# Kernel tuning notes

Hardware: AMD Instinct MI355X
Metric: run time of the kernel (lower is better)

## Reference

```python
import jax, jax.numpy as jnp
import numpy as np
from jax import lax

# ---- static config (matches init_kwargs) ----
B, D, H, HD, MLP = 64, 768, 12, 64, 3072
DEPTH = 11                     # trunk blocks; block 12 is used (twice) as b1/b2
IMG_H, IMG_W, P, S = 256, 128, 16, 12
NY, NX = (IMG_H - P) // S + 1, (IMG_W - P) // S + 1   # 21, 10
NP = NY * NX                   # 210 patches
N = NP + 1                     # +CLS = 211 tokens
NUM_CIDS = 8
SCALE = HD ** -0.5
SIE = 3.0                      # sie_xishu
SHIFT, GROUPS, DIV = 5, 2, 4
EPS = 1e-6
_PNAMES = ["ln1_g", "ln1_b", "qkv_w", "qkv_b", "proj_w", "proj_b",
           "ln2_g", "ln2_b", "fc1_w", "fc1_b", "fc2_w", "fc2_b"]


def layernorm(x, g, b):
    m = jnp.mean(x, -1, keepdims=True)
    v = jnp.mean(jnp.square(x - m), -1, keepdims=True)
    return (x - m) * lax.rsqrt(v + EPS) * g + b


def block(x, p):
    """Pre-norm ViT block: manual attention (q@k.T softmax @v) + GELU MLP."""
    ln1g, ln1b, qkvw, qkvb, projw, projb, ln2g, ln2b, fc1w, fc1b, fc2w, fc2b = p
    Bn, Nn = x.shape[0], x.shape[1]
    h = layernorm(x, ln1g, ln1b)
    qkv = (h @ qkvw + qkvb).reshape(Bn, Nn, 3, H, HD)
    q, k, v = qkv[:, :, 0], qkv[:, :, 1], qkv[:, :, 2]           # [B,N,H,HD]
    attn = jax.nn.softmax(jnp.einsum('bnhd,bmhd->bhnm', q * SCALE, k), axis=-1)
    o = jnp.einsum('bhnm,bmhd->bnhd', attn, v).reshape(Bn, Nn, D)
    x = x + o @ projw + projb
    h = layernorm(x, ln2g, ln2b)
    return x + jax.nn.gelu(h @ fc1w + fc1b, approximate=False) @ fc2w + fc2b


def _block_params(k, lead=()):
    ks = jax.random.split(k, 4)
    z = lambda s: jnp.zeros(lead + s, jnp.float32)
    o = lambda s: jnp.ones(lead + s, jnp.float32)
    r = lambda kk, s, fan: jax.random.normal(kk, lead + s, jnp.float32) * (fan ** -0.5)
    return dict(ln1_g=o((D,)), ln1_b=z((D,)),
                qkv_w=r(ks[0], (D, 3 * D), D), qkv_b=z((3 * D,)),
                proj_w=r(ks[1], (D, D), D), proj_b=z((D,)),
                ln2_g=o((D,)), ln2_b=z((D,)),
                fc1_w=r(ks[2], (D, MLP), D), fc1_b=z((MLP,)),
                fc2_w=r(ks[3], (MLP, D), MLP), fc2_b=z((D,)))


def setup_inputs() -> dict:
    key = jax.random.key(0)
    k = jax.random.split(key, 8)
    inp = {
        "x": jax.random.normal(k[0], (B, 3, IMG_H, IMG_W), jnp.float32),
        "cids": jax.random.randint(k[1], (B,), 0, NUM_CIDS),
        "conv_w": jax.random.normal(k[2], (D, 3, P, P), jnp.float32) * np.float32(np.sqrt(2.0 / (P * P * D))),
        "conv_b": jnp.zeros((D,), jnp.float32),
        "cls_token": jax.random.normal(k[3], (1, 1, D), jnp.float32) * 0.02,
        "pos_embed": jax.random.normal(k[4], (1, N, D), jnp.float32) * 0.02,
        "sie_embed": jax.random.normal(k[5], (NUM_CIDS, 1, D), jnp.float32) * 0.02,
    }
    for name, arr in _block_params(k[6], (DEPTH,)).items():
        inp["blk_" + name] = arr
    for pre, kk in (("b1_", jax.random.fold_in(key, 101)), ("b2_", jax.random.fold_in(key, 102))):
        for name, arr in _block_params(kk).items():
            inp[pre + name] = arr
        inp[pre + "norm_g"] = jnp.ones((D,), jnp.float32)
        inp[pre + "norm_b"] = jnp.zeros((D,), jnp.float32)
    return inp


def reference(x, cids, conv_w, conv_b, cls_token, pos_embed, sie_embed,
              blk_ln1_g, blk_ln1_b, blk_qkv_w, blk_qkv_b, blk_proj_w, blk_proj_b,
              blk_ln2_g, blk_ln2_b, blk_fc1_w, blk_fc1_b, blk_fc2_w, blk_fc2_b,
              b1_ln1_g, b1_ln1_b, b1_qkv_w, b1_qkv_b, b1_proj_w, b1_proj_b,
              b1_ln2_g, b1_ln2_b, b1_fc1_w, b1_fc1_b, b1_fc2_w, b1_fc2_b,
              b1_norm_g, b1_norm_b,
              b2_ln1_g, b2_ln1_b, b2_qkv_w, b2_qkv_b, b2_proj_w, b2_proj_b,
              b2_ln2_g, b2_ln2_b, b2_fc1_w, b2_fc1_b, b2_fc2_w, b2_fc2_b,
              b2_norm_g, b2_norm_b):
    Bn = x.shape[0]
    # overlapping patch embed: Conv2d(3->768, k=16, s=12), flatten, transpose
    y = lax.conv_general_dilated(x, conv_w, (S, S), 'VALID',
                                 dimension_numbers=('NCHW', 'OIHW', 'NCHW'))
    y = (y + conv_b[None, :, None, None]).reshape(Bn, D, NP).transpose(0, 2, 1)
    t = jnp.concatenate([jnp.broadcast_to(cls_token, (Bn, 1, D)), y], axis=1)
    t = t + pos_embed + SIE * sie_embed[cids]   # SIE camera embedding
    # 11 trunk blocks via scan over stacked params
    stk = (blk_ln1_g, blk_ln1_b, blk_qkv_w, blk_qkv_b, blk_proj_w, blk_proj_b,
           blk_ln2_g, blk_ln2_b, blk_fc1_w, blk_fc1_b, blk_fc2_w, blk_fc2_b)
    t = lax.scan(lambda c, p: (block(c, p), None), t, stk)[0]
    # global branch: b1 = block12 + final norm, take CLS
    b1p = (b1_ln1_g, b1_ln1_b, b1_qkv_w, b1_qkv_b, b1_proj_w, b1_proj_b,
           b1_ln2_g, b1_ln2_b, b1_fc1_w, b1_fc1_b, b1_fc2_w, b1_fc2_b)
    f0 = layernorm(block(t, b1p), b1_norm_g, b1_norm_b)[:, 0]
    # shuffle_unit(t, shift=5, group=2, begin=1) -> jigsaw rearranged patches [B,210,D]
    xs = jnp.concatenate([t[:, SHIFT:], t[:, 1:SHIFT]], axis=1)
    xs = xs.reshape(Bn, GROUPS, -1, D).transpose(0, 2, 1, 3).reshape(Bn, -1, D)
    token = t[:, 0:1]
    pl = NP // DIV                                   # 52
    b2p = (b2_ln1_g, b2_ln1_b, b2_qkv_w, b2_qkv_b, b2_proj_w, b2_proj_b,
           b2_ln2_g, b2_ln2_b, b2_fc1_w, b2_fc1_b, b2_fc2_w, b2_fc2_b)
    feats = [f0]
    for i in range(DIV):
        seg = jnp.concatenate([token, xs[:, i * pl:(i + 1) * pl]], axis=1)   # [B,53,D]
        feats.append(layernorm(block(seg, b2p), b2_norm_g, b2_norm_b)[:, 0])
    # eval output with neck_feat='before': necks pass features through;
    # concat global + local/divide_length -> [B, 5*768]
    return jnp.concatenate([feats[0]] + [f / DIV for f in feats[1:]], axis=1)
```

## Files before the change

kernel.cpp:

```cpp
#include <hip/hip_runtime.h>
#include <hip/hip_bf16.h>
#include <cstdint>
#include <cstddef>
#include <math.h>

using bf16 = __hip_bfloat16;
typedef __bf16 bf16x8 __attribute__((ext_vector_type(8)));
typedef float f32x4 __attribute__((ext_vector_type(4)));

static constexpr int NHEAD = 12;
static constexpr int NTOK  = 211;
static constexpr int DEPTH = 11;

static __device__ __forceinline__ void gload_lds16(const bf16* g, bf16* lds) {
  __builtin_amdgcn_global_load_lds(
      (const __attribute__((address_space(1))) uint32_t*)g,
      (__attribute__((address_space(3))) uint32_t*)lds,
      16, 0, 0);
}

__device__ __forceinline__ float gelu_f(float x) {
  float u = x * (0.7978845608f + 0.0356774081f * x * x);
  float t = 1.f - 2.f / (__expf(2.f * u) + 1.f);
  return 0.5f * x * (1.f + t);
}

static __device__ __forceinline__ unsigned short bf16_bits(float x) {
  return __builtin_bit_cast(unsigned short, __float2bfloat16(x));
}

template <bool GELU, bool RES, typename CT>
__global__ __launch_bounds__(256) void gemm_db(
    const bf16* __restrict__ A, const bf16* __restrict__ Bt,
    const float* __restrict__ bias, const float* __restrict__ res,
    CT* __restrict__ C, int M, int N, int K, int gn)
{
  __shared__ bf16 sb[2][8192];

  const int tid = threadIdx.x;
  const int w = tid >> 6, l = tid & 63;
  const int lr = l & 15, lg = l >> 4;
  const int wr = (w >> 1) * 64, wc = (w & 1) * 64;

  const int nwg = gridDim.x, lin = blockIdx.x;
  const int q = nwg >> 3, r = nwg & 7;
  const int xcd = lin & 7, pos = lin >> 3;
  const int wg = (xcd < r ? xcd * (q + 1) : r * (q + 1) + (xcd - r) * q) + pos;
  const int bm0 = (wg / gn) * 128, bn0 = (wg % gn) * 128;

  f32x4 acc[4][4];
#pragma unroll
  for (int i = 0; i < 4; ++i)
#pragma unroll
    for (int j = 0; j < 4; ++j) acc[i][j] = f32x4{0.f, 0.f, 0.f, 0.f};

  size_t aof[2], bof[2]; int dst[2];
#pragma unroll
  for (int j = 0; j < 2; ++j) {
    const int c = j * 256 + tid;
    const int row = c >> 2;
    const int ch = (c & 3) ^ ((row >> 1) & 3);
    int ar = bm0 + row; if (ar >= M) ar = M - 1;
    aof[j] = (size_t)ar * K + ch * 8;
    bof[j] = (size_t)(bn0 + row) * K + ch * 8;
    dst[j] = c * 8;
  }

  const int nt = K >> 5;

  auto stage = [&](int t) {
    bf16* s = sb[t & 1];
    const size_t ko = (size_t)t * 32;
    gload_lds16(A + aof[0] + ko, s + dst[0]);
    gload_lds16(A + aof[1] + ko, s + dst[1]);
    gload_lds16(Bt + bof[0] + ko, s + 4096 + dst[0]);
    gload_lds16(Bt + bof[1] + ko, s + 4096 + dst[1]);
  };

  stage(0);
  __syncthreads();

  const int swz = (lg ^ ((lr >> 1) & 3)) * 8;

  for (int t = 0; t < nt; ++t) {
    if (t + 1 < nt) stage(t + 1);
    const bf16* As = sb[t & 1];
    const bf16* Bs = As + 4096;
    bf16x8 af[4], bv[4];
#pragma unroll
    for (int mi = 0; mi < 4; ++mi)
      af[mi] = *(const bf16x8*)(As + (wr + mi * 16 + lr) * 32 + swz);
#pragma unroll
    for (int ni = 0; ni < 4; ++ni)
      bv[ni] = *(const bf16x8*)(Bs + (wc + ni * 16 + lr) * 32 + swz);
#pragma unroll
    for (int mi = 0; mi < 4; ++mi)
#pragma unroll
      for (int ni = 0; ni < 4; ++ni)
        acc[mi][ni] = __builtin_amdgcn_mfma_f32_16x16x32_bf16(af[mi], bv[ni], acc[mi][ni], 0, 0, 0);
    __syncthreads();
  }

  if constexpr (sizeof(CT) == 2) {
    char* lb = (char*)sb;
#pragma unroll
    for (int mi = 0; mi < 4; ++mi) {
#pragma unroll
      for (int ni = 0; ni < 4; ++ni) {
        const int cloc = wc + ni * 16 + lr;
        const float bvl = bias[bn0 + cloc];
#pragma unroll
        for (int r2 = 0; r2 < 4; ++r2) {
          const int rowl = wr + mi * 16 + lg * 4 + r2;
          float v = acc[mi][ni][r2] + bvl;
          if constexpr (GELU) v = gelu_f(v);
          *(unsigned short*)(lb + rowl * 256 + ((cloc * 2) ^ (((rowl >> 1) & 6) << 4))) =
              bf16_bits(v);
        }
      }
    }
    __syncthreads();
#pragma unroll
    for (int j = 0; j < 8; ++j) {
      const int flat = j * 256 + tid;
      const int row = flat >> 4, ch = flat & 15;
      const int grow = bm0 + row;
      if (grow < M) {
        const f32x4 v = *(const f32x4*)(lb + row * 256 + ((ch * 16) ^ (((row >> 1) & 6) << 4)));
        *(f32x4*)((char*)C + ((size_t)grow * N + bn0 + ch * 8) * 2) = v;
      }
    }
  } else {
#pragma unroll
    for (int mi = 0; mi < 4; ++mi) {
#pragma unroll
      for (int ni = 0; ni < 4; ++ni) {
        const int col = bn0 + wc + ni * 16 + lr;
        const float bvl = bias[col];
#pragma unroll
        for (int r2 = 0; r2 < 4; ++r2) {
          const int row = bm0 + wr + mi * 16 + lg * 4 + r2;
          if (row < M) {
            float v = acc[mi][ni][r2] + bvl;
            if constexpr (GELU) v = gelu_f(v);
            if constexpr (RES) v += res[(size_t)row * N + col];
            C[(size_t)row * N + col] = v;
          }
        }
      }
    }
  }
}

__global__ __launch_bounds__(256) void vtrans_kernel(
    const bf16* __restrict__ qkv, bf16* __restrict__ vT, int ntok, int pad)
{
  __shared__ unsigned short t[224 * 65];
  const int bb = blockIdx.x, h = blockIdx.y;
  const unsigned short* src = (const unsigned short*)qkv + (size_t)bb * ntok * 2304 + 1536 + h * 64;
  for (int idx = threadIdx.x; idx < ntok * 64; idx += 256) {
    int tok = idx >> 6, d = idx & 63;
    t[tok * 65 + d] = src[(size_t)tok * 2304 + d];
  }
  __syncthreads();
  unsigned short* dst = (unsigned short*)vT + (size_t)(bb * 12 + h) * 64 * pad;
  for (int idx = threadIdx.x; idx < 64 * ntok; idx += 256) {
    int d = idx / ntok, tok = idx - d * ntok;
    dst[(size_t)d * pad + tok] = t[tok * 65 + d];
  }
}

template <int NKF>
__global__ __launch_bounds__(256) void attn_kernel(
    const bf16* __restrict__ qkv, const bf16* __restrict__ vT,
    bf16* __restrict__ ao, int ntok, int pad)
{
  constexpr int NPAD = NKF * 16;
  __shared__ bf16 Pl[4][16][NPAD];
  const int bb = blockIdx.x;
  const int h = blockIdx.y;
  const int tid = threadIdx.x;
  const int w = tid >> 6, l = tid & 63;
  const int lr = l & 15, lg = l >> 4;
  const __bf16* base = reinterpret_cast<const __bf16*>(qkv) + (size_t)bb * ntok * 2304 + h * 64;
  const __bf16* vt = reinterpret_cast<const __bf16*>(vT) + (size_t)(bb * 12 + h) * 64 * pad;

  for (int qt = w; qt < NKF; qt += 4) {
    int qrow = qt * 16 + lr; if (qrow >= ntok) qrow = ntok - 1;
    const __bf16* qp = base + (size_t)qrow * 2304 + lg * 8;
    const bf16x8 qf0 = *reinterpret_cast<const bf16x8*>(qp);
    const bf16x8 qf1 = *reinterpret_cast<const bf16x8*>(qp + 32);

    f32x4 s[NKF];
#pragma unroll
    for (int kf = 0; kf < NKF; ++kf) {
      int krow = kf * 16 + lr; if (krow >= ntok) krow = ntok - 1;
      const __bf16* kp = base + (size_t)krow * 2304 + 768 + lg * 8;
      f32x4 a = f32x4{0.f, 0.f, 0.f, 0.f};
      a = __builtin_amdgcn_mfma_f32_16x16x32_bf16(qf0, *reinterpret_cast<const bf16x8*>(kp), a, 0, 0, 0);
      a = __builtin_amdgcn_mfma_f32_16x16x32_bf16(qf1, *reinterpret_cast<const bf16x8*>(kp + 32), a, 0, 0, 0);
      s[kf] = a;
    }

    float rs[4];
#pragma unroll
    for (int r = 0; r < 4; ++r) {
      float mx = -1e30f;
#pragma unroll
      for (int kf = 0; kf < NKF; ++kf)
        if (kf * 16 + lr < ntok) mx = fmaxf(mx, s[kf][r]);
#pragma unroll
      for (int d = 1; d < 16; d <<= 1) mx = fmaxf(mx, __shfl_xor(mx, d));
      float sum = 0.f;
#pragma unroll
      for (int kf = 0; kf < NKF; ++kf) {
        float p = 0.f;
        if (kf * 16 + lr < ntok) p = __expf((s[kf][r] - mx) * 0.125f);
        sum += p;
        Pl[w][lg * 4 + r][kf * 16 + lr] = __float2bfloat16(p);
      }
#pragma unroll
      for (int d = 1; d < 16; d <<= 1) sum += __shfl_xor(sum, d);
      rs[r] = sum;
    }
    __builtin_amdgcn_s_waitcnt(0);

    f32x4 o[4];
#pragma unroll
    for (int ni = 0; ni < 4; ++ni) o[ni] = f32x4{0.f, 0.f, 0.f, 0.f};
#pragma unroll
    for (int ks = 0; ks < NPAD / 32; ++ks) {
      const bf16x8 pa = *reinterpret_cast<const bf16x8*>(&Pl[w][lr][ks * 32 + lg * 8]);
#pragma unroll
      for (int ni = 0; ni < 4; ++ni) {
        const bf16x8 vb = *reinterpret_cast<const bf16x8*>(
            vt + (size_t)(ni * 16 + lr) * pad + ks * 32 + lg * 8);
        o[ni] = __builtin_amdgcn_mfma_f32_16x16x32_bf16(pa, vb, o[ni], 0, 0, 0);
      }
    }
#pragma unroll
    for (int ni = 0; ni < 4; ++ni)
#pragma unroll
      for (int r = 0; r < 4; ++r) {
        int qq = qt * 16 + lg * 4 + r;
        if (qq < ntok) {
          float val = o[ni][r] / rs[r];
          ao[((size_t)bb * ntok + qq) * 768 + h * 64 + ni * 16 + lr] = __float2bfloat16(val);
        }
      }
  }
}

__global__ __launch_bounds__(256) void ln_kernel(
    const float* __restrict__ x, const float* __restrict__ g, const float* __restrict__ b,
    bf16* __restrict__ out, int Mrows)
{
  int row = blockIdx.x * 4 + (threadIdx.x >> 6);
  if (row >= Mrows) return;
  int l = threadIdx.x & 63;
  const float4* xr = reinterpret_cast<const float4*>(x + (size_t)row * 768);
  float4 v[3]; float s = 0.f;
#pragma unroll
  for (int i = 0; i < 3; ++i) {
    v[i] = xr[l + i * 64];
    s += v[i].x + v[i].y + v[i].z + v[i].w;
  }
#pragma unroll
  for (int d = 1; d < 64; d <<= 1) s += __shfl_xor(s, d);
  float mean = s * (1.f / 768.f);
  float s2 = 0.f;
#pragma unroll
  for (int i = 0; i < 3; ++i) {
    float a0 = v[i].x - mean, a1 = v[i].y - mean, a2 = v[i].z - mean, a3 = v[i].w - mean;
    s2 += a0 * a0 + a1 * a1 + a2 * a2 + a3 * a3;
  }
#pragma unroll
  for (int d = 1; d < 64; d <<= 1) s2 += __shfl_xor(s2, d);
  float rstd = rsqrtf(s2 * (1.f / 768.f) + 1e-6f);
  const float4* g4 = reinterpret_cast<const float4*>(g);
  const float4* b4 = reinterpret_cast<const float4*>(b);
  unsigned short* orow = reinterpret_cast<unsigned short*>(out + (size_t)row * 768);
#pragma unroll
  for (int i = 0; i < 3; ++i) {
    float4 gg = g4[l + i * 64], bb = b4[l + i * 64];
    ushort4 pk;
    pk.x = bf16_bits((v[i].x - mean) * rstd * gg.x + bb.x);
    pk.y = bf16_bits((v[i].y - mean) * rstd * gg.y + bb.y);
    pk.z = bf16_bits((v[i].z - mean) * rstd * gg.z + bb.z);
    pk.w = bf16_bits((v[i].w - mean) * rstd * gg.w + bb.w);
    *reinterpret_cast<ushort4*>(orow + (l + i * 64) * 4) = pk;
  }
}

__global__ __launch_bounds__(256) void ln_head_kernel(
    const float* __restrict__ x, int tokstride, const float* __restrict__ g,
    const float* __restrict__ b, float* __restrict__ out, int nbb, int mode)
{
  int bb = blockIdx.x * 4 + (threadIdx.x >> 6);
  if (bb >= nbb) return;
  int l = threadIdx.x & 63;
  const float* xr = x + (size_t)bb * tokstride * 768;
  float v[12]; float s = 0.f;
#pragma unroll
  for (int i = 0; i < 12; ++i) { v[i] = xr[l + i * 64]; s += v[i]; }
#pragma unroll
  for (int d = 1; d < 64; d <<= 1) s += __shfl_xor(s, d);
  float mean = s * (1.f / 768.f);
  float s2 = 0.f;
#pragma unroll
  for (int i = 0; i < 12; ++i) { float t = v[i] - mean; s2 += t * t; }
#pragma unroll
  for (int d = 1; d < 64; d <<= 1) s2 += __shfl_xor(s2, d);
  float rstd = rsqrtf(s2 * (1.f / 768.f) + 1e-6f);
  float scale = mode ? 0.25f : 1.f;
  int b_ = mode ? (bb & 63) : bb;
  int off = mode ? (1 + (bb >> 6)) * 768 : 0;
  float* orow = out + (size_t)b_ * 3840 + off;
#pragma unroll
  for (int i = 0; i < 12; ++i) {
    orow[l + i * 64] = ((v[i] - mean) * rstd * g[l + i * 64] + b[l + i * 64]) * scale;
  }
}

__global__ __launch_bounds__(256) void transpose4_k(
    const float* __restrict__ w0, const float* __restrict__ w1,
    const float* __restrict__ w2, const float* __restrict__ w3,
    bf16* __restrict__ d0, bf16* __restrict__ d1,
    bf16* __restrict__ d2, bf16* __restrict__ d3)
{
  __shared__ float tile[32][33];
  int id = blockIdx.x;
  const float* in; bf16* out; int R, C, tt;
  if (id < 1728)      { in = w0; out = d0; R = 768;  C = 2304; tt = id; }
  else if (id < 2304) { in = w1; out = d1; R = 768;  C = 768;  tt = id - 1728; }
  else if (id < 4608) { in = w2; out = d2; R = 768;  C = 3072; tt = id - 2304; }
  else                { in = w3; out = d3; R = 3072; C = 768;  tt = id - 4608; }
  const int tc = C >> 5;
  int c0 = (tt % tc) * 32, r0 = (tt / tc) * 32;
  int tx = threadIdx.x & 31, ty = threadIdx.x >> 5;
#pragma unroll
  for (int i = 0; i < 4; ++i) {
    int rr = ty + i * 8;
    tile[rr][tx] = in[(size_t)(r0 + rr) * C + c0 + tx];
  }
  __syncthreads();
#pragma unroll
  for (int i = 0; i < 4; ++i) {
    int c = ty + i * 8;
    out[(size_t)(c0 + c) * R + r0 + tx] = __float2bfloat16(tile[tx][c]);
  }
}

__global__ void cast_kernel(const float* __restrict__ in, bf16* __restrict__ out, int n)
{
  int idx = blockIdx.x * 256 + threadIdx.x;
  if (idx < n) out[idx] = __float2bfloat16(in[idx]);
}

__global__ void im2col_kernel(const float* __restrict__ x, bf16* __restrict__ pm)
{
  int idx = blockIdx.x * 256 + threadIdx.x;
  if (idx >= 13440 * 768) return;
  int k = idx % 768;
  int m = idx / 768;
  int b = m / 210, p = m % 210;
  int py = p / 10, px = p % 10;
  int c = k >> 8, ij = k & 255, i = ij >> 4, j = ij & 15;
  pm[idx] = __float2bfloat16(x[(((size_t)b * 3 + c) * 256 + py * 12 + i) * 128 + px * 12 + j]);
}

__global__ void assemble_kernel(
    const bf16* __restrict__ y, const float* __restrict__ cls, const float* __restrict__ pos,
    const float* __restrict__ sie, const int* __restrict__ cids, float* __restrict__ tA)
{
  int idx = blockIdx.x * 256 + threadIdx.x;
  if (idx >= 13504 * 768) return;
  int d = idx % 768;
  int t = (idx / 768) % 211;
  int b = idx / (768 * 211);
  float v = pos[t * 768 + d] + 3.0f * sie[cids[b] * 768 + d];
  if (t == 0) v += cls[d];
  else v += __bfloat162float(y[((size_t)b * 210 + (t - 1)) * 768 + d]);
  tA[idx] = v;
}

__global__ void gather_kernel(const float* __restrict__ tA, float* __restrict__ tB)
{
  int idx = blockIdx.x * 256 + threadIdx.x;
  if (idx >= 256 * 53 * 768) return;
  int d = idx % 768;
  int jj = (idx / 768) % 53;
  int bb = idx / (768 * 53);
  int i = bb >> 6, b = bb & 63;
  int src;
  if (jj == 0) src = 0;
  else {
    int jx = i * 52 + (jj - 1);
    int mm = (jx & 1) * 105 + (jx >> 1);
    src = (mm < 206) ? (5 + mm) : (1 + (mm - 206));
  }
  tB[idx] = tA[((size_t)b * 211 + src) * 768 + d];
}

struct BlkP {
  const float *ln1_g, *ln1_b, *qkv_w, *qkv_b, *proj_w, *proj_b;
  const float *ln2_g, *ln2_b, *fc1_w, *fc1_b, *fc2_w, *fc2_b;
};

extern "C" void kernel_launch(void* const* d_in, const int* in_sizes, int n_in,
                              void* d_out, int out_size, void* d_ws, size_t ws_size,
                              hipStream_t stream)
{
  (void)in_sizes; (void)n_in; (void)out_size; (void)ws_size;
  const float* xin   = (const float*)d_in[0];
  const int*   cids  = (const int*)  d_in[1];
  const float* convw = (const float*)d_in[2];
  const float* convb = (const float*)d_in[3];
  const float* cls   = (const float*)d_in[4];
  const float* pos   = (const float*)d_in[5];
  const float* sie   = (const float*)d_in[6];
  float* out = (float*)d_out;

  char* ws = (char*)d_ws;
  bf16*  qkvT = (bf16*)(ws + 0);
  bf16*  projT = (bf16*)(ws + 3538944);
  bf16*  fc1T = (bf16*)(ws + 4718592);
  bf16*  fc2T = (bf16*)(ws + 9437184);
  float* tA   = (float*)(ws + 14155776);
  float* tB   = (float*)(ws + 55640064);
  bf16*  hb   = (bf16*)(ws + 97320960);
  bf16*  big  = (bf16*)(ws + 118161408);
  bf16*  ao   = (bf16*)(ws + 201523200);
  bf16*  vTb  = (bf16*)(ws + 222363648);

  dim3 blk(256);

  auto apply_block = [&](float* xbuf, const BlkP& p, int nb, int ntok_) {
    const int M = nb * ntok_;
    const int gm = (M + 127) / 128;
    const int pad = (ntok_ == NTOK) ? 224 : 64;
    transpose4_k<<<dim3(6912), blk, 0, stream>>>(
        p.qkv_w, p.proj_w, p.fc1_w, p.fc2_w, qkvT, projT, fc1T, fc2T);
    ln_kernel<<<dim3((M + 3) / 4), blk, 0, stream>>>(xbuf, p.ln1_g, p.ln1_b, hb, M);
    gemm_db<false, false, bf16><<<dim3(gm * 18), blk, 0, stream>>>(
        hb, qkvT, p.qkv_b, nullptr, big, M, 2304, 768, 18);
    vtrans_kernel<<<dim3(nb, NHEAD), blk, 0, stream>>>(big, vTb, ntok_, pad);
    if (ntok_ == NTOK)
      attn_kernel<14><<<dim3(nb, NHEAD), blk, 0, stream>>>(big, vTb, ao, ntok_, pad);
    else
      attn_kernel<4><<<dim3(nb, NHEAD), blk, 0, stream>>>(big, vTb, ao, ntok_, pad);
    gemm_db<false, true, float><<<dim3(gm * 6), blk, 0, stream>>>(
        ao, projT, p.proj_b, xbuf, xbuf, M, 768, 768, 6);
    ln_kernel<<<dim3((M + 3) / 4), blk, 0, stream>>>(xbuf, p.ln2_g, p.ln2_b, hb, M);
    gemm_db<true, false, bf16><<<dim3(gm * 24), blk, 0, stream>>>(
        hb, fc1T, p.fc1_b, nullptr, big, M, 3072, 768, 24);
    gemm_db<false, true, float><<<dim3(gm * 6), blk, 0, stream>>>(
        big, fc2T, p.fc2_b, xbuf, xbuf, M, 768, 3072, 6);
  };

  {
    int total = 13440 * 768;
    im2col_kernel<<<dim3((total + 255) / 256), blk, 0, stream>>>(xin, big);
    int nw = 768 * 768;
    cast_kernel<<<dim3((nw + 255) / 256), blk, 0, stream>>>(convw, qkvT, nw);
    gemm_db<false, false, bf16><<<dim3(105 * 6), blk, 0, stream>>>(
        big, qkvT, convb, nullptr, ao, 13440, 768, 768, 6);
    total = 13504 * 768;
    assemble_kernel<<<dim3((total + 255) / 256), blk, 0, stream>>>(ao, cls, pos, sie, cids, tA);
  }

  const float* bp[12];
  for (int i = 0; i < 12; ++i) bp[i] = (const float*)d_in[7 + i];
  for (int dd = 0; dd < DEPTH; ++dd) {
    BlkP p;
    p.ln1_g = bp[0] + dd * 768;                p.ln1_b = bp[1] + dd * 768;
    p.qkv_w = bp[2] + (size_t)dd * 768 * 2304; p.qkv_b = bp[3] + dd * 2304;
    p.proj_w = bp[4] + (size_t)dd * 768 * 768; p.proj_b = bp[5] + dd * 768;
    p.ln2_g = bp[6] + dd * 768;                p.ln2_b = bp[7] + dd * 768;
    p.fc1_w = bp[8] + (size_t)dd * 768 * 3072; p.fc1_b = bp[9] + dd * 3072;
    p.fc2_w = bp[10] + (size_t)dd * 3072 * 768; p.fc2_b = bp[11] + dd * 768;
    apply_block(tA, p, 64, NTOK);
  }

  (void)hipMemcpyAsync(tB, tA, (size_t)13504 * 768 * 4, hipMemcpyDeviceToDevice, stream);
  {
    BlkP p;
    p.ln1_g = (const float*)d_in[19]; p.ln1_b = (const float*)d_in[20];
    p.qkv_w = (const float*)d_in[21]; p.qkv_b = (const float*)d_in[22];
    p.proj_w = (const float*)d_in[23]; p.proj_b = (const float*)d_in[24];
    p.ln2_g = (const float*)d_in[25]; p.ln2_b = (const float*)d_in[26];
    p.fc1_w = (const float*)d_in[27]; p.fc1_b = (const float*)d_in[28];
    p.fc2_w = (const float*)d_in[29]; p.fc2_b = (const float*)d_in[30];
    apply_block(tB, p, 64, NTOK);
    ln_head_kernel<<<dim3(16), blk, 0, stream>>>(
        tB, NTOK, (const float*)d_in[31], (const float*)d_in[32], out, 64, 0);
  }

  {
    int total = 256 * 53 * 768;
    gather_kernel<<<dim3((total + 255) / 256), blk, 0, stream>>>(tA, tB);
    BlkP p;
    p.ln1_g = (const float*)d_in[33]; p.ln1_b = (const float*)d_in[34];
    p.qkv_w = (const float*)d_in[35]; p.qkv_b = (const float*)d_in[36];
    p.proj_w = (const float*)d_in[37]; p.proj_b = (const float*)d_in[38];
    p.ln2_g = (const float*)d_in[39]; p.ln2_b = (const float*)d_in[40];
    p.fc1_w = (const float*)d_in[41]; p.fc1_b = (const float*)d_in[42];
    p.fc2_w = (const float*)d_in[43]; p.fc2_b = (const float*)d_in[44];
    apply_block(tB, p, 256, 53);
    ln_head_kernel<<<dim3(64), blk, 0, stream>>>(
        tB, 53, (const float*)d_in[45], (const float*)d_in[46], out, 256, 1);
  }
}
```

Measured before the change: 5.550 ms.

## Add wide 128x256 bf16 GEMM with LDS-staged epilogue for QKV and FC1

```diff
diff --git a/kernel.cpp b/kernel.cpp
--- a/kernel.cpp
+++ b/kernel.cpp
@@ -149,6 +149,122 @@
         }
       }
     }
+  }
+}
+
+template <bool GELU>
+__global__ __launch_bounds__(256, 2) void gemm_dw(
+    const bf16* __restrict__ A, const bf16* __restrict__ Bt,
+    const float* __restrict__ bias, bf16* __restrict__ C,
+    int M, int N, int K, int gn)
+{
+  __shared__ bf16 sb[2][12288];
+
+  const int tid = threadIdx.x;
+  const int w = tid >> 6, l = tid & 63;
+  const int lr = l & 15, lg = l >> 4;
+  const int wr = (w >> 1) * 64;
+  const int wc = (w & 1) * 128;
+
+  const int nwg = gridDim.x, lin = blockIdx.x;
+  const int q = nwg >> 3, r = nwg & 7;
+  const int xcd = lin & 7, pos = lin >> 3;
+  const int wg = (xcd < r ? xcd * (q + 1) : r * (q + 1) + (xcd - r) * q) + pos;
+  const int bm0 = (wg / gn) * 128, bn0 = (wg % gn) * 256;
+
+  f32x4 acc[4][8];
+#pragma unroll
+  for (int i = 0; i < 4; ++i)
+#pragma unroll
+    for (int j = 0; j < 8; ++j) acc[i][j] = f32x4{0.f, 0.f, 0.f, 0.f};
+
+  unsigned aofs[2], bofs[4];
+#pragma unroll
+  for (int j = 0; j < 2; ++j) {
+    const int c = j * 256 + tid;
+    const int row = c >> 2;
+    const int ch = (c & 3) ^ ((row >> 1) & 3);
+    int ar = bm0 + row; if (ar >= M) ar = M - 1;
+    aofs[j] = (unsigned)(ar * K + ch * 8);
+  }
+#pragma unroll
+  for (int j = 0; j < 4; ++j) {
+    const int c = j * 256 + tid;
+    const int row = c >> 2;
+    const int ch = (c & 3) ^ ((row >> 1) & 3);
+    bofs[j] = (unsigned)((bn0 + row) * K + ch * 8);
+  }
+
+  const int nt = K >> 5;
+
+  auto stage = [&](int t) {
+    bf16* s = sb[t & 1];
+    const unsigned ko = (unsigned)t * 32;
+#pragma unroll
+    for (int j = 0; j < 2; ++j)
+      gload_lds16(A + aofs[j] + ko, s + (j * 256 + tid) * 8);
+#pragma unroll
+    for (int j = 0; j < 4; ++j)
+      gload_lds16(Bt + bofs[j] + ko, s + 4096 + (j * 256 + tid) * 8);
+  };
+
+  stage(0);
+  __syncthreads();
+
+  const int swz = (lg ^ ((lr >> 1) & 3)) * 8;
+
+  for (int t = 0; t < nt; ++t) {
+    if (t + 1 < nt) stage(t + 1);
+    const bf16* As = sb[t & 1];
+    const bf16* Bs = As + 4096;
+    bf16x8 af[4], bv[8];
+#pragma unroll
+    for (int mi = 0; mi < 4; ++mi)
+      af[mi] = *(const bf16x8*)(As + (wr + mi * 16 + lr) * 32 + swz);
+#pragma unroll
+    for (int ni = 0; ni < 8; ++ni)
+      bv[ni] = *(const bf16x8*)(Bs + (wc + ni * 16 + lr) * 32 + swz);
+#pragma unroll
+    for (int mi = 0; mi < 4; ++mi)
+#pragma unroll
+      for (int ni = 0; ni < 8; ++ni)
+        acc[mi][ni] = __builtin_amdgcn_mfma_f32_16x16x32_bf16(af[mi], bv[ni], acc[mi][ni], 0, 0, 0);
+    __syncthreads();
+  }
+
+  char* lb = (char*)sb;
+#pragma unroll
+  for (int hh = 0; hh < 2; ++hh) {
+    if ((w & 1) == hh) {
+#pragma unroll
+      for (int mi = 0; mi < 4; ++mi) {
+#pragma unroll
+        for (int ni = 0; ni < 8; ++ni) {
+          const int cloc = ni * 16 + lr;
+          const float bvl = bias[bn0 + hh * 128 + cloc];
+#pragma unroll
+          for (int r2 = 0; r2 < 4; ++r2) {
+            const int rowl = wr + mi * 16 + lg * 4 + r2;
+            float v = acc[mi][ni][r2] + bvl;
+            if constexpr (GELU) v = gelu_f(v);
+            *(unsigned short*)(lb + rowl * 256 + ((cloc * 2) ^ (((rowl >> 1) & 6) << 4))) =
+                bf16_bits(v);
+          }
+        }
+      }
+    }
+    __syncthreads();
+#pragma unroll
+    for (int j = 0; j < 8; ++j) {
+      const int flat = j * 256 + tid;
+      const int row = flat >> 4, ch = flat & 15;
+      const int grow = bm0 + row;
+      if (grow < M) {
+        const f32x4 v = *(const f32x4*)(lb + row * 256 + ((ch * 16) ^ (((row >> 1) & 6) << 4)));
+        *(f32x4*)((char*)C + ((size_t)grow * N + bn0 + hh * 128 + ch * 8) * 2) = v;
+      }
+    }
+    __syncthreads();
   }
 }
 
@@ -442,8 +558,8 @@
     transpose4_k<<<dim3(6912), blk, 0, stream>>>(
         p.qkv_w, p.proj_w, p.fc1_w, p.fc2_w, qkvT, projT, fc1T, fc2T);
     ln_kernel<<<dim3((M + 3) / 4), blk, 0, stream>>>(xbuf, p.ln1_g, p.ln1_b, hb, M);
-    gemm_db<false, false, bf16><<<dim3(gm * 18), blk, 0, stream>>>(
-        hb, qkvT, p.qkv_b, nullptr, big, M, 2304, 768, 18);
+    gemm_dw<false><<<dim3(gm * 9), blk, 0, stream>>>(
+        hb, qkvT, p.qkv_b, big, M, 2304, 768, 9);
     vtrans_kernel<<<dim3(nb, NHEAD), blk, 0, stream>>>(big, vTb, ntok_, pad);
     if (ntok_ == NTOK)
       attn_kernel<14><<<dim3(nb, NHEAD), blk, 0, stream>>>(big, vTb, ao, ntok_, pad);
@@ -452,8 +568,8 @@
     gemm_db<false, true, float><<<dim3(gm * 6), blk, 0, stream>>>(
         ao, projT, p.proj_b, xbuf, xbuf, M, 768, 768, 6);
     ln_kernel<<<dim3((M + 3) / 4), blk, 0, stream>>>(xbuf, p.ln2_g, p.ln2_b, hb, M);
-    gemm_db<true, false, bf16><<<dim3(gm * 24), blk, 0, stream>>>(
-        hb, fc1T, p.fc1_b, nullptr, big, M, 3072, 768, 24);
+    gemm_dw<true><<<dim3(gm * 12), blk, 0, stream>>>(
+        hb, fc1T, p.fc1_b, big, M, 3072, 768, 12);
     gemm_db<false, true, float><<<dim3(gm * 6), blk, 0, stream>>>(
         big, fc2T, p.fc2_b, xbuf, xbuf, M, 768, 3072, 6);
   };
```

Result: no change. 5.630 ms (+1.4%).

## Compute head blocks only for CLS token after attention

Applied to the files above, without the earlier changes.

```diff
diff --git a/kernel.cpp b/kernel.cpp
--- a/kernel.cpp
+++ b/kernel.cpp
@@ -33,7 +33,7 @@
 __global__ __launch_bounds__(256) void gemm_db(
     const bf16* __restrict__ A, const bf16* __restrict__ Bt,
     const float* __restrict__ bias, const float* __restrict__ res,
-    CT* __restrict__ C, int M, int N, int K, int gn)
+    CT* __restrict__ C, int M, int N, int K, int gn, int sA, int sR, int sC)
 {
   __shared__ bf16 sb[2][8192];
 
@@ -61,7 +61,7 @@
     const int row = c >> 2;
     const int ch = (c & 3) ^ ((row >> 1) & 3);
     int ar = bm0 + row; if (ar >= M) ar = M - 1;
-    aof[j] = (size_t)ar * K + ch * 8;
+    aof[j] = (size_t)ar * sA + ch * 8;
     bof[j] = (size_t)(bn0 + row) * K + ch * 8;
     dst[j] = c * 8;
   }
@@ -127,7 +127,7 @@
       const int grow = bm0 + row;
       if (grow < M) {
         const f32x4 v = *(const f32x4*)(lb + row * 256 + ((ch * 16) ^ (((row >> 1) & 6) << 4)));
-        *(f32x4*)((char*)C + ((size_t)grow * N + bn0 + ch * 8) * 2) = v;
+        *(f32x4*)((char*)C + ((size_t)grow * sC + bn0 + ch * 8) * 2) = v;
       }
     }
   } else {
@@ -143,8 +143,8 @@
           if (row < M) {
             float v = acc[mi][ni][r2] + bvl;
             if constexpr (GELU) v = gelu_f(v);
-            if constexpr (RES) v += res[(size_t)row * N + col];
-            C[(size_t)row * N + col] = v;
+            if constexpr (RES) v += res[(size_t)row * sR + col];
+            C[(size_t)row * sC + col] = v;
           }
         }
       }
@@ -170,7 +170,7 @@
   }
 }
 
-template <int NKF>
+template <int NKF, bool ONLY0>
 __global__ __launch_bounds__(256) void attn_kernel(
     const bf16* __restrict__ qkv, const bf16* __restrict__ vT,
     bf16* __restrict__ ao, int ntok, int pad)
@@ -182,10 +182,11 @@
   const int tid = threadIdx.x;
   const int w = tid >> 6, l = tid & 63;
   const int lr = l & 15, lg = l >> 4;
+  if (ONLY0 && w > 0) return;
   const __bf16* base = reinterpret_cast<const __bf16*>(qkv) + (size_t)bb * ntok * 2304 + h * 64;
   const __bf16* vt = reinterpret_cast<const __bf16*>(vT) + (size_t)(bb * 12 + h) * 64 * pad;
 
-  for (int qt = w; qt < NKF; qt += 4) {
+  for (int qt = w; qt < (ONLY0 ? 1 : NKF); qt += 4) {
     int qrow = qt * 16 + lr; if (qrow >= ntok) qrow = ntok - 1;
     const __bf16* qp = base + (size_t)qrow * 2304 + lg * 8;
     const bf16x8 qf0 = *reinterpret_cast<const bf16x8*>(qp);
@@ -243,7 +244,7 @@
 #pragma unroll
       for (int r = 0; r < 4; ++r) {
         int qq = qt * 16 + lg * 4 + r;
-        if (qq < ntok) {
+        if (qq < (ONLY0 ? 1 : ntok)) {
           float val = o[ni][r] / rs[r];
           ao[((size_t)bb * ntok + qq) * 768 + h * 64 + ni * 16 + lr] = __float2bfloat16(val);
         }
@@ -432,6 +433,11 @@
   bf16*  big  = (bf16*)(ws + 118161408);
   bf16*  ao   = (bf16*)(ws + 201523200);
   bf16*  vTb  = (bf16*)(ws + 222363648);
+  char*  sbuf = ws + 118161408 + 73400320;
+  float* y0   = (float*)(sbuf);
+  bf16*  hb0  = (bf16*)(sbuf + 786432);
+  bf16*  big0 = (bf16*)(sbuf + 1179648);
+  float* f0b  = (float*)(sbuf + 2752512);
 
   dim3 blk(256);
 
@@ -443,19 +449,44 @@
         p.qkv_w, p.proj_w, p.fc1_w, p.fc2_w, qkvT, projT, fc1T, fc2T);
     ln_kernel<<<dim3((M + 3) / 4), blk, 0, stream>>>(xbuf, p.ln1_g, p.ln1_b, hb, M);
     gemm_db<false, false, bf16><<<dim3(gm * 18), blk, 0, stream>>>(
-        hb, qkvT, p.qkv_b, nullptr, big, M, 2304, 768, 18);
+        hb, qkvT, p.qkv_b, nullptr, big, M, 2304, 768, 18, 768, 2304, 2304);
+    vtrans_kernel<<<dim3(nb, NHEAD), blk, 0, stream>>>(big, vTb, ntok_, pad);
+    attn_kernel<14, false><<<dim3(nb, NHEAD), blk, 0, stream>>>(big, vTb, ao, ntok_, pad);
+    gemm_db<false, true, float><<<dim3(gm * 6), blk, 0, stream>>>(
+        ao, projT, p.proj_b, xbuf, xbuf, M, 768, 768, 6, 768, 768, 768);
+    ln_kernel<<<dim3((M + 3) / 4), blk, 0, stream>>>(xbuf, p.ln2_g, p.ln2_b, hb, M);
+    gemm_db<true, false, bf16><<<dim3(gm * 24), blk, 0, stream>>>(
+        hb, fc1T, p.fc1_b, nullptr, big, M, 3072, 768, 24, 768, 3072, 3072);
+    gemm_db<false, true, float><<<dim3(gm * 6), blk, 0, stream>>>(
+        big, fc2T, p.fc2_b, xbuf, xbuf, M, 768, 3072, 6, 3072, 768, 768);
+  };
+
+  auto apply_head_block = [&](const float* xsrc, const BlkP& p, int nb, int ntok_,
+                              const float* ng, const float* nbias, int mode) {
+    const int M = nb * ntok_;
+    const int gm = (M + 127) / 128;
+    const int gm0 = (nb + 127) / 128;
+    const int pad = (ntok_ == NTOK) ? 224 : 64;
+    const int ts = ntok_ * 768;
+    transpose4_k<<<dim3(6912), blk, 0, stream>>>(
+        p.qkv_w, p.proj_w, p.fc1_w, p.fc2_w, qkvT, projT, fc1T, fc2T);
+    ln_kernel<<<dim3((M + 3) / 4), blk, 0, stream>>>(xsrc, p.ln1_g, p.ln1_b, hb, M);
+    gemm_db<false, false, bf16><<<dim3(gm * 18), blk, 0, stream>>>(
+        hb, qkvT, p.qkv_b, nullptr, big, M, 2304, 768, 18, 768, 2304, 2304);
     vtrans_kernel<<<dim3(nb, NHEAD), blk, 0, stream>>>(big, vTb, ntok_, pad);
     if (ntok_ == NTOK)
-      attn_kernel<14><<<dim3(nb, NHEAD), blk, 0, stream>>>(big, vTb, ao, ntok_, pad);
+      attn_kernel<14, true><<<dim3(nb, NHEAD), blk, 0, stream>>>(big, vTb, ao, ntok_, pad);
     else
-      attn_kernel<4><<<dim3(nb, NHEAD), blk, 0, stream>>>(big, vTb, ao, ntok_, pad);
-    gemm_db<false, true, float><<<dim3(gm * 6), blk, 0, stream>>>(
-        ao, projT, p.proj_b, xbuf, xbuf, M, 768, 768, 6);
-    ln_kernel<<<dim3((M + 3) / 4), blk, 0, stream>>>(xbuf, p.ln2_g, p.ln2_b, hb, M);
-    gemm_db<true, false, bf16><<<dim3(gm * 24), blk, 0, stream>>>(
-        hb, fc1T, p.fc1_b, nullptr, big, M, 3072, 768, 24);
-    gemm_db<false, true, float><<<dim3(gm * 6), blk, 0, stream>>>(
-        big, fc2T, p.fc2_b, xbuf, xbuf, M, 768, 3072, 6);
+      attn_kernel<4, true><<<dim3(nb, NHEAD), blk, 0, stream>>>(big, vTb, ao, ntok_, pad);
+    gemm_db<false, true, float><<<dim3(gm0 * 6), blk, 0, stream>>>(
+        ao, projT, p.proj_b, xsrc, y0, nb, 768, 768, 6, ts, ts, 768);
+    ln_kernel<<<dim3((nb + 3) / 4), blk, 0, stream>>>(y0, p.ln2_g, p.ln2_b, hb0, nb);
+    gemm_db<true, false, bf16><<<dim3(gm0 * 24), blk, 0, stream>>>(
+        hb0, fc1T, p.fc1_b, nullptr, big0, nb, 3072, 768, 24, 768, 3072, 3072);
+    gemm_db<false, true, float><<<dim3(gm0 * 6), blk, 0, stream>>>(
+        big0, fc2T, p.fc2_b, y0, f0b, nb, 768, 3072, 6, 3072, 768, 768);
+    ln_head_kernel<<<dim3((nb + 3) / 4), blk, 0, stream>>>(
+        f0b, 1, ng, nbias, out, nb, mode);
   };
 
   {
@@ -464,7 +495,7 @@
     int nw = 768 * 768;
     cast_kernel<<<dim3((nw + 255) / 256), blk, 0, stream>>>(convw, qkvT, nw);
     gemm_db<false, false, bf16><<<dim3(105 * 6), blk, 0, stream>>>(
-        big, qkvT, convb, nullptr, ao, 13440, 768, 768, 6);
+        big, qkvT, convb, nullptr, ao, 13440, 768, 768, 6, 768, 768, 768);
     total = 13504 * 768;
     assemble_kernel<<<dim3((total + 255) / 256), blk, 0, stream>>>(ao, cls, pos, sie, cids, tA);
   }
@@ -482,7 +513,6 @@
     apply_block(tA, p, 64, NTOK);
   }
 
-  (void)hipMemcpyAsync(tB, tA, (size_t)13504 * 768 * 4, hipMemcpyDeviceToDevice, stream);
   {
     BlkP p;
     p.ln1_g = (const float*)d_in[19]; p.ln1_b = (const float*)d_in[20];
@@ -491,9 +521,8 @@
     p.ln2_g = (const float*)d_in[25]; p.ln2_b = (const float*)d_in[26];
     p.fc1_w = (const float*)d_in[27]; p.fc1_b = (const float*)d_in[28];
     p.fc2_w = (const float*)d_in[29]; p.fc2_b = (const float*)d_in[30];
-    apply_block(tB, p, 64, NTOK);
-    ln_head_kernel<<<dim3(16), blk, 0, stream>>>(
-        tB, NTOK, (const float*)d_in[31], (const float*)d_in[32], out, 64, 0);
+    apply_head_block(tA, p, 64, NTOK,
+                     (const float*)d_in[31], (const float*)d_in[32], 0);
   }
 
   {
@@ -506,8 +535,7 @@
     p.ln2_g = (const float*)d_in[39]; p.ln2_b = (const float*)d_in[40];
     p.fc1_w = (const float*)d_in[41]; p.fc1_b = (const float*)d_in[42];
     p.fc2_w = (const float*)d_in[43]; p.fc2_b = (const float*)d_in[44];
-    apply_block(tB, p, 256, 53);
-    ln_head_kernel<<<dim3(64), blk, 0, stream>>>(
-        tB, 53, (const float*)d_in[45], (const float*)d_in[46], out, 256, 1);
-  }
-}
+    apply_head_block(tB, p, 256, 53,
+                     (const float*)d_in[45], (const float*)d_in[46], 1);
+  }
+}
```

Measured after the change: 5.167 ms. 1.07x faster.
